# Kernel optimization log

Measured on AMD Instinct MI355X. Metric: run time of the kernel, lower is better.

## Reference

```python
import jax, jax.numpy as jnp
import numpy as np

SPLIT = 8            # square window (split_size=[8,8], idx 0/1 identical)
DIM = 192
HEADS = 8
NH = HEADS // 2      # heads per branch
CH = DIM // 2        # channels per branch
HD = CH // NH        # head dim = 24
POS_DIM = (CH // 4) // 4  # DynamicPosBias hidden = 6
SCALE = HD ** -0.5
N = SPLIT * SPLIT    # window token count = 64


def _rel_index():
    c = np.arange(SPLIT)
    coords = np.stack(np.meshgrid(c, c, indexing='ij')).reshape(2, -1)
    rel = (coords[:, :, None] - coords[:, None, :]).transpose(1, 2, 0)
    rel[:, :, 0] += SPLIT - 1
    rel[:, :, 1] += SPLIT - 1
    rel[:, :, 0] *= 2 * SPLIT - 1
    return rel.sum(-1).reshape(-1)  # (N*N,) in [0, (2*SPLIT-1)^2)


def _rpe_biases():
    h = np.arange(1 - SPLIT, SPLIT)
    b = np.stack(np.meshgrid(h, h, indexing='ij')).reshape(2, -1).T
    return b.astype(np.float32)  # ((2*SPLIT-1)^2, 2) = (225, 2)


def _layernorm(x, g, b):
    mu = x.mean(-1, keepdims=True)
    var = ((x - mu) ** 2).mean(-1, keepdims=True)
    return (x - mu) / jnp.sqrt(var + 1e-5) * g + b


def setup_inputs() -> dict:
    key = jax.random.key(0)
    ks = jax.random.split(key, 12)
    s = 0.02
    inp = {
        'x': jax.random.normal(ks[0], (2, 65536, DIM), jnp.float32),
        'qkv_w': jax.random.normal(ks[1], (3 * DIM, DIM), jnp.float32) * s,
        'proj_w': jax.random.normal(ks[2], (DIM, DIM), jnp.float32) * s,
        'proj_b': jnp.zeros((DIM,), jnp.float32),
        # DynamicPosBias params, stacked over the 2 branches
        'pos_proj_w': jax.random.normal(ks[3], (2, POS_DIM, 2), jnp.float32) * s,
        'pos_proj_b': jnp.zeros((2, POS_DIM), jnp.float32),
        'ln1_g': jnp.ones((2, POS_DIM), jnp.float32),
        'ln1_b': jnp.zeros((2, POS_DIM), jnp.float32),
        'fc1_w': jax.random.normal(ks[4], (2, POS_DIM, POS_DIM), jnp.float32) * s,
        'fc1_b': jnp.zeros((2, POS_DIM), jnp.float32),
        'ln2_g': jnp.ones((2, POS_DIM), jnp.float32),
        'ln2_b': jnp.zeros((2, POS_DIM), jnp.float32),
        'fc2_w': jax.random.normal(ks[5], (2, POS_DIM, POS_DIM), jnp.float32) * s,
        'fc2_b': jnp.zeros((2, POS_DIM), jnp.float32),
        'ln3_g': jnp.ones((2, POS_DIM), jnp.float32),
        'ln3_b': jnp.zeros((2, POS_DIM), jnp.float32),
        'fc3_w': jax.random.normal(ks[6], (2, NH, POS_DIM), jnp.float32) * s,
        'fc3_b': jnp.zeros((2, NH), jnp.float32),
        'H': 256,
        'W': 256,
    }
    return inp


def reference(x, qkv_w, proj_w, proj_b, pos_proj_w, pos_proj_b,
              ln1_g, ln1_b, fc1_w, fc1_b, ln2_g, ln2_b, fc2_w, fc2_b,
              ln3_g, ln3_b, fc3_w, fc3_b, H, W):
    B, L, C = x.shape
    assert L == H * W and H % SPLIT == 0 and W % SPLIT == 0
    qkv = (x @ qkv_w.T).reshape(B, L, 3, C).transpose(2, 0, 1, 3)  # (3,B,L,C)
    rel_idx = jnp.asarray(_rel_index())
    rpe = jnp.asarray(_rpe_biases())
    outs = []
    for i in range(2):  # two channel-split branches
        qkv_i = qkv[..., i * CH:(i + 1) * CH]  # (3,B,L,CH)
        # window partition: (B,L,CH) -> (B*nW, NH, N, HD)
        def im2win(t):
            t = t.reshape(B, H // SPLIT, SPLIT, W // SPLIT, SPLIT, CH)
            t = t.transpose(0, 1, 3, 2, 4, 5).reshape(-1, N, NH, HD)
            return t.transpose(0, 2, 1, 3)
        q, k, v = im2win(qkv_i[0]), im2win(qkv_i[1]), im2win(qkv_i[2])
        attn = jnp.einsum('whnd,whmd->whnm', q * SCALE, k)  # (B*nW, NH, N, N)
        # dynamic relative position bias MLP (residual=False): pos3(pos2(pos1(proj(b))))
        pos = rpe @ pos_proj_w[i].T + pos_proj_b[i]
        pos = jax.nn.relu(_layernorm(pos, ln1_g[i], ln1_b[i])) @ fc1_w[i].T + fc1_b[i]
        pos = jax.nn.relu(_layernorm(pos, ln2_g[i], ln2_b[i])) @ fc2_w[i].T + fc2_b[i]
        pos = jax.nn.relu(_layernorm(pos, ln3_g[i], ln3_b[i])) @ fc3_w[i].T + fc3_b[i]  # (225, NH)
        bias = pos[rel_idx].reshape(N, N, NH).transpose(2, 0, 1)  # (NH, N, N)
        attn = jax.nn.softmax(attn + bias[None], axis=-1)
        o = jnp.einsum('whnm,whmd->whnd', attn, v)  # (B*nW, NH, N, HD)
        # windows2img back to (B, L, CH)
        o = o.transpose(0, 2, 1, 3).reshape(B, H // SPLIT, W // SPLIT, SPLIT, SPLIT, CH)
        o = o.transpose(0, 1, 3, 2, 4, 5).reshape(B, L, CH)
        outs.append(o)
    out = jnp.concatenate(outs, axis=-1)
    return out @ proj_w.T + proj_b
```

## Files before the change

### kernel.cpp

```cpp
#include <hip/hip_runtime.h>

typedef unsigned short u16;
typedef short short8v __attribute__((ext_vector_type(8)));
typedef float float4v __attribute__((ext_vector_type(4)));
typedef unsigned short ushort4v __attribute__((ext_vector_type(4)));

#define XLD   216
#define C1LD  392
#define VSLD  72
#define PLD   72
#define VS_OFF (64*C1LD)
#define LDS_U16 (VS_OFF + 8*24*VSLD)
#define LDS_BYTES (LDS_U16*2)

__device__ __forceinline__ u16 f2bf(float f){
  unsigned u = __builtin_bit_cast(unsigned, f);
  return (u16)((u + 0x7FFFu + ((u >> 16) & 1u)) >> 16);
}

__global__ void prep_convert(const float* __restrict__ qkv_w, const float* __restrict__ proj_w,
                             u16* __restrict__ Wq, u16* __restrict__ Wp){
  int idx = blockIdx.x*blockDim.x + threadIdx.x;
  const int total = 110592 + 36864;
  for (; idx < total; idx += gridDim.x*blockDim.x){
    if (idx < 110592) Wq[idx] = f2bf(qkv_w[idx]);
    else              Wp[idx-110592] = f2bf(proj_w[idx-110592]);
  }
}

__device__ __forceinline__ void lnrelu6(float* v, const float* g, const float* b){
  float mu = (v[0]+v[1]+v[2]+v[3]+v[4]+v[5]) * (1.0f/6.0f);
  float var = 0.f;
  #pragma unroll
  for (int j=0;j<6;++j){ float d = v[j]-mu; var += d*d; }
  var *= (1.0f/6.0f);
  float inv = rsqrtf(var + 1e-5f);
  #pragma unroll
  for (int j=0;j<6;++j) v[j] = fmaxf((v[j]-mu)*inv*g[j] + b[j], 0.f);
}

__global__ void prep_bias(const float* __restrict__ ppw, const float* __restrict__ ppb,
                          const float* __restrict__ ln1g, const float* __restrict__ ln1b,
                          const float* __restrict__ fc1w, const float* __restrict__ fc1b,
                          const float* __restrict__ ln2g, const float* __restrict__ ln2b,
                          const float* __restrict__ fc2w, const float* __restrict__ fc2b,
                          const float* __restrict__ ln3g, const float* __restrict__ ln3b,
                          const float* __restrict__ fc3w, const float* __restrict__ fc3b,
                          float* __restrict__ biasT){
  __shared__ float pos3[2][225][4];
  const int t = threadIdx.x;
  if (t < 225){
    const float dy = (float)(t/15) - 7.0f;
    const float dx = (float)(t%15) - 7.0f;
    for (int i=0;i<2;++i){
      float v[6], y[6];
      #pragma unroll
      for (int j=0;j<6;++j)
        v[j] = dy*ppw[(i*6+j)*2+0] + dx*ppw[(i*6+j)*2+1] + ppb[i*6+j];
      lnrelu6(v, ln1g+i*6, ln1b+i*6);
      #pragma unroll
      for (int j=0;j<6;++j){
        float a = fc1b[i*6+j];
        #pragma unroll
        for (int k=0;k<6;++k) a += v[k]*fc1w[(i*6+j)*6+k];
        y[j] = a;
      }
      lnrelu6(y, ln2g+i*6, ln2b+i*6);
      #pragma unroll
      for (int j=0;j<6;++j){
        float a = fc2b[i*6+j];
        #pragma unroll
        for (int k=0;k<6;++k) a += y[k]*fc2w[(i*6+j)*6+k];
        v[j] = a;
      }
      lnrelu6(v, ln3g+i*6, ln3b+i*6);
      #pragma unroll
      for (int h=0;h<4;++h){
        float a = fc3b[i*4+h];
        #pragma unroll
        for (int k=0;k<6;++k) a += v[k]*fc3w[(i*4+h)*6+k];
        pos3[i][t][h] = a;
      }
    }
  }
  __syncthreads();
  for (int idx = t; idx < 32768; idx += 256){
    int i  = idx >> 14;
    int hh = (idx >> 12) & 3;
    int n  = (idx >> 6) & 63;
    int m  = idx & 63;
    int tt = (((n>>3)-(m>>3)+7)*15) + ((n&7)-(m&7)+7);
    biasT[idx] = pos3[i][tt][hh];
  }
}

__global__ __launch_bounds__(256, 2) void awa_main(
    const float* __restrict__ x, const u16* __restrict__ Wq,
    const u16* __restrict__ Wp, const float* __restrict__ proj_b,
    const float* __restrict__ biasT, float* __restrict__ out){
  extern __shared__ u16 lds[];
  const int tid  = threadIdx.x;
  const int wave = tid >> 6;
  const int lane = tid & 63;
  const int g    = lane >> 4;
  const int q16  = lane & 15;
  const int bid  = blockIdx.x;
  const int b    = bid >> 10;
  const int win  = bid & 1023;
  const int h1   = win >> 5, w1 = win & 31;
  const size_t xbase = ((size_t)b*65536u + (size_t)(h1*8)*256u + (size_t)(w1*8)) * 192u;
  const short8v z8 = {0,0,0,0,0,0,0,0};

  #pragma unroll
  for (int it = 0; it < 12; ++it){
    int fi  = tid + it*256;
    int f   = fi << 2;
    int rr  = f / 1536;
    int rem = f - rr*1536;
    int ss  = rem / 192;
    int cc  = rem - ss*192;
    float4v xv = *(const float4v*)(x + xbase + (size_t)((rr*256 + ss)*192 + cc));
    ushort4v pk = { f2bf(xv[0]), f2bf(xv[1]), f2bf(xv[2]), f2bf(xv[3]) };
    *(ushort4v*)&lds[(rr*8+ss)*XLD + cc] = pk;
  }
  __syncthreads();

  short8v xf[4][6];
  #pragma unroll
  for (int mt=0; mt<4; ++mt)
    #pragma unroll
    for (int kc=0; kc<6; ++kc)
      xf[mt][kc] = *(const short8v*)&lds[(mt*16+q16)*XLD + kc*32 + g*8];
  short8v wf[2][6];
  {
    const u16* wb = Wq + (size_t)(wave*16 + q16)*192 + g*8;
    #pragma unroll
    for (int kc=0;kc<6;++kc) wf[0][kc] = *(const short8v*)(wb + kc*32);
  }
  __syncthreads();

  #pragma unroll
  for (int t=0; t<9; ++t){
    const int nt = wave + t*4;
    if (t < 8){
      const u16* wb = Wq + (size_t)((nt+4)*16 + q16)*192 + g*8;
      #pragma unroll
      for (int kc=0;kc<6;++kc) wf[(t+1)&1][kc] = *(const short8v*)(wb + kc*32);
    }
    float4v acc[4];
    #pragma unroll
    for (int mt=0;mt<4;++mt) acc[mt] = (float4v){0.f,0.f,0.f,0.f};
    if (t < 6){
      #pragma unroll
      for (int kc=0; kc<6; ++kc)
        #pragma unroll
        for (int mt=0; mt<4; ++mt)
          acc[mt] = __builtin_amdgcn_mfma_f32_16x16x32_bf16(wf[t&1][kc], xf[mt][kc], acc[mt], 0,0,0);
      const int cb = nt*16 + g*4;
      #pragma unroll
      for (int mt=0; mt<4; ++mt){
        ushort4v pk = { f2bf(acc[mt][0]), f2bf(acc[mt][1]), f2bf(acc[mt][2]), f2bf(acc[mt][3]) };
        *(ushort4v*)&lds[(mt*16+q16)*C1LD + cb] = pk;
      }
    } else {
      #pragma unroll
      for (int kc=0; kc<6; ++kc)
        #pragma unroll
        for (int mt=0; mt<4; ++mt)
          acc[mt] = __builtin_amdgcn_mfma_f32_16x16x32_bf16(xf[mt][kc], wf[t&1][kc], acc[mt], 0,0,0);
      const int jj  = nt*16 + q16 - 384;
      const int ii2 = (jj >= 96) ? 1 : 0;
      const int c2  = jj - ii2*96;
      const int hh2 = c2 / 24;
      const int d   = c2 - hh2*24;
      const int vb  = VS_OFF + ((ii2*4 + hh2)*24 + d)*VSLD + g*4;
      #pragma unroll
      for (int mt=0; mt<4; ++mt){
        ushort4v pk = { f2bf(acc[mt][0]), f2bf(acc[mt][1]), f2bf(acc[mt][2]), f2bf(acc[mt][3]) };
        *(ushort4v*)&lds[vb + mt*16] = pk;
      }
    }
  }
  __syncthreads();

  short8v qf[2][4], kf[2][4];
  #pragma unroll
  for (int h=0; h<2; ++h){
    const int qb = h*96 + wave*24;
    #pragma unroll
    for (int mt=0; mt<4; ++mt){
      short8v a = *(const short8v*)&lds[(mt*16+q16)*C1LD + qb + g*8];
      short8v c = *(const short8v*)&lds[(mt*16+q16)*C1LD + 192 + qb + g*8];
      qf[h][mt] = (g==3) ? z8 : a;
      kf[h][mt] = (g==3) ? z8 : c;
    }
  }
  __syncthreads();

  u16* P = &lds[wave*4608];
  float4v oo[2][2][4];
  #pragma unroll
  for (int h=0; h<2; ++h){
    const int hp = h*4 + wave;
    float4v s[4][4];
    #pragma unroll
    for (int kt=0;kt<4;++kt)
      #pragma unroll
      for (int mt=0;mt<4;++mt)
        s[kt][mt] = (float4v){0.f,0.f,0.f,0.f};
    #pragma unroll
    for (int kt=0;kt<4;++kt)
      #pragma unroll
      for (int mt=0;mt<4;++mt)
        s[kt][mt] = __builtin_amdgcn_mfma_f32_16x16x32_bf16(kf[h][kt], qf[h][mt], s[kt][mt], 0,0,0);
    const float* bt = biasT + hp*4096;
    #pragma unroll
    for (int kt=0;kt<4;++kt)
      #pragma unroll
      for (int mt=0;mt<4;++mt){
        float4v bv = *(const float4v*)&bt[(mt*16+q16)*64 + kt*16 + g*4];
        s[kt][mt] = s[kt][mt]*0.20412414523193154f + bv;
      }
    #pragma unroll
    for (int mt=0;mt<4;++mt){
      float mx = s[0][mt][0];
      #pragma unroll
      for (int kt=0;kt<4;++kt)
        #pragma unroll
        for (int r=0;r<4;++r) mx = fmaxf(mx, s[kt][mt][r]);
      mx = fmaxf(mx, __shfl_xor(mx, 16));
      mx = fmaxf(mx, __shfl_xor(mx, 32));
      float e[4][4]; float sum = 0.f;
      #pragma unroll
      for (int kt=0;kt<4;++kt)
        #pragma unroll
        for (int r=0;r<4;++r){ float t2 = __expf(s[kt][mt][r]-mx); e[kt][r] = t2; sum += t2; }
      sum += __shfl_xor(sum, 16);
      sum += __shfl_xor(sum, 32);
      const float inv = 1.0f / sum;
      #pragma unroll
      for (int kt=0;kt<4;++kt){
        ushort4v pk = { f2bf(e[kt][0]*inv), f2bf(e[kt][1]*inv), f2bf(e[kt][2]*inv), f2bf(e[kt][3]*inv) };
        *(ushort4v*)&P[(mt*16+q16)*PLD + kt*16 + g*4] = pk;
      }
    }
    short8v vf[2][2];
    #pragma unroll
    for (int dt=0;dt<2;++dt){
      const int d  = dt*16 + q16;
      const int dc = (d < 24) ? d : 0;
      #pragma unroll
      for (int kc=0;kc<2;++kc){
        short8v vv = *(const short8v*)&lds[VS_OFF + (hp*24 + dc)*VSLD + kc*32 + g*8];
        vf[dt][kc] = (d < 24) ? vv : z8;
      }
    }
    #pragma unroll
    for (int dt=0;dt<2;++dt)
      #pragma unroll
      for (int mt=0;mt<4;++mt) oo[h][dt][mt] = (float4v){0.f,0.f,0.f,0.f};
    #pragma unroll
    for (int mt=0;mt<4;++mt){
      #pragma unroll
      for (int kc=0;kc<2;++kc){
        short8v pf = *(const short8v*)&P[(mt*16+q16)*PLD + kc*32 + g*8];
        #pragma unroll
        for (int dt=0;dt<2;++dt)
          oo[h][dt][mt] = __builtin_amdgcn_mfma_f32_16x16x32_bf16(vf[dt][kc], pf, oo[h][dt][mt], 0,0,0);
      }
    }
  }
  __syncthreads();

  #pragma unroll
  for (int h=0; h<2; ++h){
    const int cb = h*96 + wave*24;
    #pragma unroll
    for (int dt=0; dt<2; ++dt){
      if (dt==0 || g<2){
        #pragma unroll
        for (int mt=0; mt<4; ++mt){
          ushort4v pk = { f2bf(oo[h][dt][mt][0]), f2bf(oo[h][dt][mt][1]),
                          f2bf(oo[h][dt][mt][2]), f2bf(oo[h][dt][mt][3]) };
          *(ushort4v*)&lds[(mt*16+q16)*XLD + cb + dt*16 + g*4] = pk;
        }
      }
    }
  }
  short8v wp[2][6];
  {
    const u16* wb = Wp + (size_t)(wave*16 + q16)*192 + g*8;
    #pragma unroll
    for (int kc=0;kc<6;++kc) wp[0][kc] = *(const short8v*)(wb + kc*32);
  }
  __syncthreads();

  short8v a2[4][6];
  #pragma unroll
  for (int mt=0; mt<4; ++mt)
    #pragma unroll
    for (int kc=0; kc<6; ++kc)
      a2[mt][kc] = *(const short8v*)&lds[(mt*16+q16)*XLD + kc*32 + g*8];
  #pragma unroll
  for (int t=0; t<3; ++t){
    const int nt = wave + t*4;
    if (t < 2){
      const u16* wb = Wp + (size_t)((nt+4)*16 + q16)*192 + g*8;
      #pragma unroll
      for (int kc=0;kc<6;++kc) wp[(t+1)&1][kc] = *(const short8v*)(wb + kc*32);
    }
    float4v acc[4];
    #pragma unroll
    for (int mt=0;mt<4;++mt) acc[mt] = (float4v){0.f,0.f,0.f,0.f};
    #pragma unroll
    for (int kc=0; kc<6; ++kc)
      #pragma unroll
      for (int mt=0; mt<4; ++mt)
        acc[mt] = __builtin_amdgcn_mfma_f32_16x16x32_bf16(wp[t&1][kc], a2[mt][kc], acc[mt], 0,0,0);
    const int j0 = nt*16 + g*4;
    const float4v pb = *(const float4v*)(proj_b + j0);
    #pragma unroll
    for (int mt=0; mt<4; ++mt){
      const int tok = mt*16 + q16;
      const int l = ((h1*8 + (tok>>3)) << 8) + w1*8 + (tok & 7);
      float4v res = acc[mt] + pb;
      *(float4v*)(out + ((size_t)b*65536u + (size_t)l)*192u + j0) = res;
    }
  }
}

extern "C" void kernel_launch(void* const* d_in, const int* in_sizes, int n_in,
                              void* d_out, int out_size, void* d_ws, size_t ws_size,
                              hipStream_t stream){
  const float* x      = (const float*)d_in[0];
  const float* qkv_w  = (const float*)d_in[1];
  const float* proj_w = (const float*)d_in[2];
  const float* proj_b = (const float*)d_in[3];
  const float* ppw    = (const float*)d_in[4];
  const float* ppb    = (const float*)d_in[5];
  const float* ln1g   = (const float*)d_in[6];
  const float* ln1b   = (const float*)d_in[7];
  const float* fc1w   = (const float*)d_in[8];
  const float* fc1b   = (const float*)d_in[9];
  const float* ln2g   = (const float*)d_in[10];
  const float* ln2b   = (const float*)d_in[11];
  const float* fc2w   = (const float*)d_in[12];
  const float* fc2b   = (const float*)d_in[13];
  const float* ln3g   = (const float*)d_in[14];
  const float* ln3b   = (const float*)d_in[15];
  const float* fc3w   = (const float*)d_in[16];
  const float* fc3b   = (const float*)d_in[17];

  u16*   Wq    = (u16*)d_ws;
  u16*   Wp    = Wq + 110592;
  float* biasT = (float*)((char*)d_ws + 294912);

  prep_convert<<<144, 256, 0, stream>>>(qkv_w, proj_w, Wq, Wp);
  prep_bias<<<1, 256, 0, stream>>>(ppw, ppb, ln1g, ln1b, fc1w, fc1b,
                                   ln2g, ln2b, fc2w, fc2b, ln3g, ln3b,
                                   fc3w, fc3b, biasT);
  awa_main<<<2048, 256, LDS_BYTES, stream>>>(x, Wq, Wp, proj_b, biasT, (float*)d_out);
}
```

Baseline: 143.1 us.

## Use eight waves per window block, one head per wave, with MFMA priority hints

Result: slower. 196.4 us (+37.2%).

```diff
diff --git a/kernel.cpp b/kernel.cpp
--- a/kernel.cpp
+++ b/kernel.cpp
@@ -94,7 +94,7 @@
   }
 }
 
-__global__ __launch_bounds__(256, 2) void awa_main(
+__global__ __launch_bounds__(512, 4) void awa_main(
     const float* __restrict__ x, const u16* __restrict__ Wq,
     const u16* __restrict__ Wp, const float* __restrict__ proj_b,
     const float* __restrict__ biasT, float* __restrict__ out){
@@ -104,6 +104,8 @@
   const int lane = tid & 63;
   const int g    = lane >> 4;
   const int q16  = lane & 15;
+  const int mh   = wave & 1;
+  const int ng   = wave >> 1;
   const int bid  = blockIdx.x;
   const int b    = bid >> 10;
   const int win  = bid & 1023;
@@ -112,8 +114,8 @@
   const short8v z8 = {0,0,0,0,0,0,0,0};
 
   #pragma unroll
-  for (int it = 0; it < 12; ++it){
-    int fi  = tid + it*256;
+  for (int it = 0; it < 6; ++it){
+    int fi  = tid + it*512;
     int f   = fi << 2;
     int rr  = f / 1536;
     int rem = f - rr*1536;
@@ -125,15 +127,15 @@
   }
   __syncthreads();
 
-  short8v xf[4][6];
-  #pragma unroll
-  for (int mt=0; mt<4; ++mt)
+  short8v xf[2][6];
+  #pragma unroll
+  for (int mi=0; mi<2; ++mi)
     #pragma unroll
     for (int kc=0; kc<6; ++kc)
-      xf[mt][kc] = *(const short8v*)&lds[(mt*16+q16)*XLD + kc*32 + g*8];
+      xf[mi][kc] = *(const short8v*)&lds[((mh*2+mi)*16+q16)*XLD + kc*32 + g*8];
   short8v wf[2][6];
   {
-    const u16* wb = Wq + (size_t)(wave*16 + q16)*192 + g*8;
+    const u16* wb = Wq + (size_t)(ng*16 + q16)*192 + g*8;
     #pragma unroll
     for (int kc=0;kc<6;++kc) wf[0][kc] = *(const short8v*)(wb + kc*32);
   }
@@ -141,33 +143,33 @@
 
   #pragma unroll
   for (int t=0; t<9; ++t){
-    const int nt = wave + t*4;
+    const int nt = ng + t*4;
     if (t < 8){
       const u16* wb = Wq + (size_t)((nt+4)*16 + q16)*192 + g*8;
       #pragma unroll
       for (int kc=0;kc<6;++kc) wf[(t+1)&1][kc] = *(const short8v*)(wb + kc*32);
     }
-    float4v acc[4];
-    #pragma unroll
-    for (int mt=0;mt<4;++mt) acc[mt] = (float4v){0.f,0.f,0.f,0.f};
+    float4v acc[2];
+    acc[0] = (float4v){0.f,0.f,0.f,0.f};
+    acc[1] = (float4v){0.f,0.f,0.f,0.f};
     if (t < 6){
       #pragma unroll
       for (int kc=0; kc<6; ++kc)
         #pragma unroll
-        for (int mt=0; mt<4; ++mt)
-          acc[mt] = __builtin_amdgcn_mfma_f32_16x16x32_bf16(wf[t&1][kc], xf[mt][kc], acc[mt], 0,0,0);
+        for (int mi=0; mi<2; ++mi)
+          acc[mi] = __builtin_amdgcn_mfma_f32_16x16x32_bf16(wf[t&1][kc], xf[mi][kc], acc[mi], 0,0,0);
       const int cb = nt*16 + g*4;
       #pragma unroll
-      for (int mt=0; mt<4; ++mt){
-        ushort4v pk = { f2bf(acc[mt][0]), f2bf(acc[mt][1]), f2bf(acc[mt][2]), f2bf(acc[mt][3]) };
-        *(ushort4v*)&lds[(mt*16+q16)*C1LD + cb] = pk;
+      for (int mi=0; mi<2; ++mi){
+        ushort4v pk = { f2bf(acc[mi][0]), f2bf(acc[mi][1]), f2bf(acc[mi][2]), f2bf(acc[mi][3]) };
+        *(ushort4v*)&lds[((mh*2+mi)*16+q16)*C1LD + cb] = pk;
       }
     } else {
       #pragma unroll
       for (int kc=0; kc<6; ++kc)
         #pragma unroll
-        for (int mt=0; mt<4; ++mt)
-          acc[mt] = __builtin_amdgcn_mfma_f32_16x16x32_bf16(xf[mt][kc], wf[t&1][kc], acc[mt], 0,0,0);
+        for (int mi=0; mi<2; ++mi)
+          acc[mi] = __builtin_amdgcn_mfma_f32_16x16x32_bf16(xf[mi][kc], wf[t&1][kc], acc[mi], 0,0,0);
       const int jj  = nt*16 + q16 - 384;
       const int ii2 = (jj >= 96) ? 1 : 0;
       const int c2  = jj - ii2*96;
@@ -175,44 +177,53 @@
       const int d   = c2 - hh2*24;
       const int vb  = VS_OFF + ((ii2*4 + hh2)*24 + d)*VSLD + g*4;
       #pragma unroll
-      for (int mt=0; mt<4; ++mt){
-        ushort4v pk = { f2bf(acc[mt][0]), f2bf(acc[mt][1]), f2bf(acc[mt][2]), f2bf(acc[mt][3]) };
-        *(ushort4v*)&lds[vb + mt*16] = pk;
-      }
-    }
-  }
-  __syncthreads();
-
-  short8v qf[2][4], kf[2][4];
-  #pragma unroll
-  for (int h=0; h<2; ++h){
-    const int qb = h*96 + wave*24;
-    #pragma unroll
-    for (int mt=0; mt<4; ++mt){
-      short8v a = *(const short8v*)&lds[(mt*16+q16)*C1LD + qb + g*8];
-      short8v c = *(const short8v*)&lds[(mt*16+q16)*C1LD + 192 + qb + g*8];
-      qf[h][mt] = (g==3) ? z8 : a;
-      kf[h][mt] = (g==3) ? z8 : c;
+      for (int mi=0; mi<2; ++mi){
+        ushort4v pk = { f2bf(acc[mi][0]), f2bf(acc[mi][1]), f2bf(acc[mi][2]), f2bf(acc[mi][3]) };
+        *(ushort4v*)&lds[vb + (mh*2+mi)*16] = pk;
+      }
+    }
+  }
+  __syncthreads();
+
+  const int hp = wave;
+  const int qb = (hp>>2)*96 + (hp&3)*24;
+  short8v qf[4], kf[4];
+  #pragma unroll
+  for (int mt=0; mt<4; ++mt){
+    short8v a = *(const short8v*)&lds[(mt*16+q16)*C1LD + qb + g*8];
+    short8v c = *(const short8v*)&lds[(mt*16+q16)*C1LD + 192 + qb + g*8];
+    qf[mt] = (g==3) ? z8 : a;
+    kf[mt] = (g==3) ? z8 : c;
+  }
+  short8v vf[2][2];
+  #pragma unroll
+  for (int dt=0;dt<2;++dt){
+    const int d  = dt*16 + q16;
+    const int dc = (d < 24) ? d : 0;
+    #pragma unroll
+    for (int kc=0;kc<2;++kc){
+      short8v vv = *(const short8v*)&lds[VS_OFF + (hp*24 + dc)*VSLD + kc*32 + g*8];
+      vf[dt][kc] = (d < 24) ? vv : z8;
     }
   }
   __syncthreads();
 
   u16* P = &lds[wave*4608];
-  float4v oo[2][2][4];
-  #pragma unroll
-  for (int h=0; h<2; ++h){
-    const int hp = h*4 + wave;
+  float4v oo[2][4];
+  {
     float4v s[4][4];
     #pragma unroll
     for (int kt=0;kt<4;++kt)
       #pragma unroll
       for (int mt=0;mt<4;++mt)
         s[kt][mt] = (float4v){0.f,0.f,0.f,0.f};
+    __builtin_amdgcn_s_setprio(1);
     #pragma unroll
     for (int kt=0;kt<4;++kt)
       #pragma unroll
       for (int mt=0;mt<4;++mt)
-        s[kt][mt] = __builtin_amdgcn_mfma_f32_16x16x32_bf16(kf[h][kt], qf[h][mt], s[kt][mt], 0,0,0);
+        s[kt][mt] = __builtin_amdgcn_mfma_f32_16x16x32_bf16(kf[kt], qf[mt], s[kt][mt], 0,0,0);
+    __builtin_amdgcn_s_setprio(0);
     const float* bt = biasT + hp*4096;
     #pragma unroll
     for (int kt=0;kt<4;++kt)
@@ -244,86 +255,79 @@
         *(ushort4v*)&P[(mt*16+q16)*PLD + kt*16 + g*4] = pk;
       }
     }
-    short8v vf[2][2];
-    #pragma unroll
-    for (int dt=0;dt<2;++dt){
-      const int d  = dt*16 + q16;
-      const int dc = (d < 24) ? d : 0;
-      #pragma unroll
-      for (int kc=0;kc<2;++kc){
-        short8v vv = *(const short8v*)&lds[VS_OFF + (hp*24 + dc)*VSLD + kc*32 + g*8];
-        vf[dt][kc] = (d < 24) ? vv : z8;
-      }
-    }
     #pragma unroll
     for (int dt=0;dt<2;++dt)
       #pragma unroll
-      for (int mt=0;mt<4;++mt) oo[h][dt][mt] = (float4v){0.f,0.f,0.f,0.f};
+      for (int mt=0;mt<4;++mt) oo[dt][mt] = (float4v){0.f,0.f,0.f,0.f};
     #pragma unroll
     for (int mt=0;mt<4;++mt){
       #pragma unroll
       for (int kc=0;kc<2;++kc){
         short8v pf = *(const short8v*)&P[(mt*16+q16)*PLD + kc*32 + g*8];
+        __builtin_amdgcn_s_setprio(1);
         #pragma unroll
         for (int dt=0;dt<2;++dt)
-          oo[h][dt][mt] = __builtin_amdgcn_mfma_f32_16x16x32_bf16(vf[dt][kc], pf, oo[h][dt][mt], 0,0,0);
-      }
-    }
-  }
-  __syncthreads();
-
-  #pragma unroll
-  for (int h=0; h<2; ++h){
-    const int cb = h*96 + wave*24;
+          oo[dt][mt] = __builtin_amdgcn_mfma_f32_16x16x32_bf16(vf[dt][kc], pf, oo[dt][mt], 0,0,0);
+        __builtin_amdgcn_s_setprio(0);
+      }
+    }
+  }
+  __syncthreads();
+
+  {
+    const int cb = qb;
     #pragma unroll
     for (int dt=0; dt<2; ++dt){
       if (dt==0 || g<2){
         #pragma unroll
         for (int mt=0; mt<4; ++mt){
-          ushort4v pk = { f2bf(oo[h][dt][mt][0]), f2bf(oo[h][dt][mt][1]),
-                          f2bf(oo[h][dt][mt][2]), f2bf(oo[h][dt][mt][3]) };
+          ushort4v pk = { f2bf(oo[dt][mt][0]), f2bf(oo[dt][mt][1]),
+                          f2bf(oo[dt][mt][2]), f2bf(oo[dt][mt][3]) };
           *(ushort4v*)&lds[(mt*16+q16)*XLD + cb + dt*16 + g*4] = pk;
         }
       }
     }
   }
+  const int nq = wave >> 1;
   short8v wp[2][6];
   {
-    const u16* wb = Wp + (size_t)(wave*16 + q16)*192 + g*8;
+    const u16* wb = Wp + (size_t)(nq*16 + q16)*192 + g*8;
     #pragma unroll
     for (int kc=0;kc<6;++kc) wp[0][kc] = *(const short8v*)(wb + kc*32);
   }
   __syncthreads();
 
-  short8v a2[4][6];
-  #pragma unroll
-  for (int mt=0; mt<4; ++mt)
+  short8v a2[2][6];
+  #pragma unroll
+  for (int mi=0; mi<2; ++mi)
     #pragma unroll
     for (int kc=0; kc<6; ++kc)
-      a2[mt][kc] = *(const short8v*)&lds[(mt*16+q16)*XLD + kc*32 + g*8];
+      a2[mi][kc] = *(const short8v*)&lds[((mh*2+mi)*16+q16)*XLD + kc*32 + g*8];
   #pragma unroll
   for (int t=0; t<3; ++t){
-    const int nt = wave + t*4;
+    const int nt = nq + t*4;
     if (t < 2){
       const u16* wb = Wp + (size_t)((nt+4)*16 + q16)*192 + g*8;
       #pragma unroll
       for (int kc=0;kc<6;++kc) wp[(t+1)&1][kc] = *(const short8v*)(wb + kc*32);
     }
-    float4v acc[4];
-    #pragma unroll
-    for (int mt=0;mt<4;++mt) acc[mt] = (float4v){0.f,0.f,0.f,0.f};
+    float4v acc[2];
+    acc[0] = (float4v){0.f,0.f,0.f,0.f};
+    acc[1] = (float4v){0.f,0.f,0.f,0.f};
+    __builtin_amdgcn_s_setprio(1);
     #pragma unroll
     for (int kc=0; kc<6; ++kc)
       #pragma unroll
-      for (int mt=0; mt<4; ++mt)
-        acc[mt] = __builtin_amdgcn_mfma_f32_16x16x32_bf16(wp[t&1][kc], a2[mt][kc], acc[mt], 0,0,0);
+      for (int mi=0; mi<2; ++mi)
+        acc[mi] = __builtin_amdgcn_mfma_f32_16x16x32_bf16(wp[t&1][kc], a2[mi][kc], acc[mi], 0,0,0);
+    __builtin_amdgcn_s_setprio(0);
     const int j0 = nt*16 + g*4;
     const float4v pb = *(const float4v*)(proj_b + j0);
     #pragma unroll
-    for (int mt=0; mt<4; ++mt){
-      const int tok = mt*16 + q16;
+    for (int mi=0; mi<2; ++mi){
+      const int tok = (mh*2+mi)*16 + q16;
       const int l = ((h1*8 + (tok>>3)) << 8) + w1*8 + (tok & 7);
-      float4v res = acc[mt] + pb;
+      float4v res = acc[mi] + pb;
       *(float4v*)(out + ((size_t)b*65536u + (size_t)l)*192u + j0) = res;
     }
   }
@@ -359,5 +363,5 @@
   prep_bias<<<1, 256, 0, stream>>>(ppw, ppb, ln1g, ln1b, fc1w, fc1b,
                                    ln2g, ln2b, fc2w, fc2b, ln3g, ln3b,
                                    fc3w, fc3b, biasT);
-  awa_main<<<2048, 256, LDS_BYTES, stream>>>(x, Wq, Wp, proj_b, biasT, (float*)d_out);
-}
+  awa_main<<<2048, 512, LDS_BYTES, stream>>>(x, Wq, Wp, proj_b, biasT, (float*)d_out);
+}
```

## Process four windows per block with register prefetch of next window input

Applied to the files above, without the earlier changes.

New measurement: 224.7 us. 1.57x slower.

```diff
diff --git a/kernel.cpp b/kernel.cpp
--- a/kernel.cpp
+++ b/kernel.cpp
@@ -12,6 +12,9 @@
 #define VS_OFF (64*C1LD)
 #define LDS_U16 (VS_OFF + 8*24*VSLD)
 #define LDS_BYTES (LDS_U16*2)
+
+#define SOFT_BAR() do { asm volatile("s_waitcnt lgkmcnt(0)" ::: "memory"); \
+                        __builtin_amdgcn_s_barrier(); } while(0)
 
 __device__ __forceinline__ u16 f2bf(float f){
   unsigned u = __builtin_bit_cast(unsigned, f);
@@ -94,6 +97,81 @@
   }
 }
 
+__device__ __forceinline__ void attn_head(u16* lds, u16* P, const float* bt,
+                                          const short8v* qf, const short8v* kf,
+                                          const float4v* bv, int hp, int q16, int g,
+                                          float4v (&oo)[2][4]){
+  const short8v z8 = {0,0,0,0,0,0,0,0};
+  float4v s[4][4];
+  #pragma unroll
+  for (int kt=0;kt<4;++kt)
+    #pragma unroll
+    for (int mt=0;mt<4;++mt)
+      s[kt][mt] = (float4v){0.f,0.f,0.f,0.f};
+  __builtin_amdgcn_s_setprio(1);
+  #pragma unroll
+  for (int kt=0;kt<4;++kt)
+    #pragma unroll
+    for (int mt=0;mt<4;++mt)
+      s[kt][mt] = __builtin_amdgcn_mfma_f32_16x16x32_bf16(kf[kt], qf[mt], s[kt][mt], 0,0,0);
+  __builtin_amdgcn_s_setprio(0);
+  #pragma unroll
+  for (int kt=0;kt<4;++kt)
+    #pragma unroll
+    for (int mt=0;mt<4;++mt)
+      s[kt][mt] = s[kt][mt]*0.20412414523193154f + bv[kt*4+mt];
+  #pragma unroll
+  for (int mt=0;mt<4;++mt){
+    float mx = s[0][mt][0];
+    #pragma unroll
+    for (int kt=0;kt<4;++kt)
+      #pragma unroll
+      for (int r=0;r<4;++r) mx = fmaxf(mx, s[kt][mt][r]);
+    mx = fmaxf(mx, __shfl_xor(mx, 16));
+    mx = fmaxf(mx, __shfl_xor(mx, 32));
+    float e[4][4]; float sum = 0.f;
+    #pragma unroll
+    for (int kt=0;kt<4;++kt)
+      #pragma unroll
+      for (int r=0;r<4;++r){ float t2 = __expf(s[kt][mt][r]-mx); e[kt][r] = t2; sum += t2; }
+    sum += __shfl_xor(sum, 16);
+    sum += __shfl_xor(sum, 32);
+    const float inv = 1.0f / sum;
+    #pragma unroll
+    for (int kt=0;kt<4;++kt){
+      ushort4v pk = { f2bf(e[kt][0]*inv), f2bf(e[kt][1]*inv), f2bf(e[kt][2]*inv), f2bf(e[kt][3]*inv) };
+      *(ushort4v*)&P[(mt*16+q16)*PLD + kt*16 + g*4] = pk;
+    }
+  }
+  short8v vf[2][2];
+  #pragma unroll
+  for (int dt=0;dt<2;++dt){
+    const int d  = dt*16 + q16;
+    const int dc = (d < 24) ? d : 0;
+    #pragma unroll
+    for (int kc=0;kc<2;++kc){
+      short8v vv = *(const short8v*)&lds[VS_OFF + (hp*24 + dc)*VSLD + kc*32 + g*8];
+      vf[dt][kc] = (d < 24) ? vv : z8;
+    }
+  }
+  #pragma unroll
+  for (int dt=0;dt<2;++dt)
+    #pragma unroll
+    for (int mt=0;mt<4;++mt) oo[dt][mt] = (float4v){0.f,0.f,0.f,0.f};
+  #pragma unroll
+  for (int mt=0;mt<4;++mt){
+    #pragma unroll
+    for (int kc=0;kc<2;++kc){
+      short8v pf = *(const short8v*)&P[(mt*16+q16)*PLD + kc*32 + g*8];
+      __builtin_amdgcn_s_setprio(1);
+      #pragma unroll
+      for (int dt=0;dt<2;++dt)
+        oo[dt][mt] = __builtin_amdgcn_mfma_f32_16x16x32_bf16(vf[dt][kc], pf, oo[dt][mt], 0,0,0);
+      __builtin_amdgcn_s_setprio(0);
+    }
+  }
+}
+
 __global__ __launch_bounds__(256, 2) void awa_main(
     const float* __restrict__ x, const u16* __restrict__ Wq,
     const u16* __restrict__ Wp, const float* __restrict__ proj_b,
@@ -104,228 +182,202 @@
   const int lane = tid & 63;
   const int g    = lane >> 4;
   const int q16  = lane & 15;
-  const int bid  = blockIdx.x;
-  const int b    = bid >> 10;
-  const int win  = bid & 1023;
-  const int h1   = win >> 5, w1 = win & 31;
-  const size_t xbase = ((size_t)b*65536u + (size_t)(h1*8)*256u + (size_t)(w1*8)) * 192u;
   const short8v z8 = {0,0,0,0,0,0,0,0};
 
-  #pragma unroll
-  for (int it = 0; it < 12; ++it){
-    int fi  = tid + it*256;
-    int f   = fi << 2;
-    int rr  = f / 1536;
-    int rem = f - rr*1536;
-    int ss  = rem / 192;
-    int cc  = rem - ss*192;
-    float4v xv = *(const float4v*)(x + xbase + (size_t)((rr*256 + ss)*192 + cc));
-    ushort4v pk = { f2bf(xv[0]), f2bf(xv[1]), f2bf(xv[2]), f2bf(xv[3]) };
-    *(ushort4v*)&lds[(rr*8+ss)*XLD + cc] = pk;
-  }
-  __syncthreads();
-
-  short8v xf[4][6];
-  #pragma unroll
-  for (int mt=0; mt<4; ++mt)
-    #pragma unroll
-    for (int kc=0; kc<6; ++kc)
-      xf[mt][kc] = *(const short8v*)&lds[(mt*16+q16)*XLD + kc*32 + g*8];
-  short8v wf[2][6];
+  float4v xr[12];
+  int gw = blockIdx.x*4;
   {
-    const u16* wb = Wq + (size_t)(wave*16 + q16)*192 + g*8;
-    #pragma unroll
-    for (int kc=0;kc<6;++kc) wf[0][kc] = *(const short8v*)(wb + kc*32);
-  }
-  __syncthreads();
-
-  #pragma unroll
-  for (int t=0; t<9; ++t){
-    const int nt = wave + t*4;
-    if (t < 8){
-      const u16* wb = Wq + (size_t)((nt+4)*16 + q16)*192 + g*8;
-      #pragma unroll
-      for (int kc=0;kc<6;++kc) wf[(t+1)&1][kc] = *(const short8v*)(wb + kc*32);
-    }
-    float4v acc[4];
-    #pragma unroll
-    for (int mt=0;mt<4;++mt) acc[mt] = (float4v){0.f,0.f,0.f,0.f};
-    if (t < 6){
+    const int b0 = gw >> 10, win0 = gw & 1023;
+    const size_t xb = ((size_t)b0*65536u + (size_t)((win0>>5)*8)*256u + (size_t)((win0&31)*8)) * 192u;
+    #pragma unroll
+    for (int it=0; it<12; ++it){
+      int f = (tid + it*256) << 2;
+      int rr = f/1536, rem = f - rr*1536, ss = rem/192, cc = rem - ss*192;
+      xr[it] = *(const float4v*)(x + xb + (size_t)((rr*256+ss)*192+cc));
+    }
+  }
+
+  for (int wloc = 0; wloc < 4; ++wloc){
+    const int b   = gw >> 10;
+    const int win = gw & 1023;
+    const int h1  = win >> 5, w1 = win & 31;
+
+    #pragma unroll
+    for (int it=0; it<12; ++it){
+      int f = (tid + it*256) << 2;
+      int rr = f/1536, rem = f - rr*1536, ss = rem/192, cc = rem - ss*192;
+      ushort4v pk = { f2bf(xr[it][0]), f2bf(xr[it][1]), f2bf(xr[it][2]), f2bf(xr[it][3]) };
+      *(ushort4v*)&lds[(rr*8+ss)*XLD + cc] = pk;
+    }
+    SOFT_BAR();
+
+    short8v xf[4][6];
+    #pragma unroll
+    for (int mt=0; mt<4; ++mt)
       #pragma unroll
       for (int kc=0; kc<6; ++kc)
+        xf[mt][kc] = *(const short8v*)&lds[(mt*16+q16)*XLD + kc*32 + g*8];
+    short8v wf[2][6];
+    {
+      const u16* wb = Wq + (size_t)(wave*16 + q16)*192 + g*8;
+      #pragma unroll
+      for (int kc=0;kc<6;++kc) wf[0][kc] = *(const short8v*)(wb + kc*32);
+    }
+    SOFT_BAR();
+
+    #pragma unroll
+    for (int t=0; t<9; ++t){
+      const int nt = wave + t*4;
+      if (t < 8){
+        const u16* wb = Wq + (size_t)((nt+4)*16 + q16)*192 + g*8;
+        #pragma unroll
+        for (int kc=0;kc<6;++kc) wf[(t+1)&1][kc] = *(const short8v*)(wb + kc*32);
+      }
+      float4v acc[4];
+      #pragma unroll
+      for (int mt=0;mt<4;++mt) acc[mt] = (float4v){0.f,0.f,0.f,0.f};
+      if (t < 6){
+        #pragma unroll
+        for (int kc=0; kc<6; ++kc)
+          #pragma unroll
+          for (int mt=0; mt<4; ++mt)
+            acc[mt] = __builtin_amdgcn_mfma_f32_16x16x32_bf16(wf[t&1][kc], xf[mt][kc], acc[mt], 0,0,0);
+        const int cb = nt*16 + g*4;
+        #pragma unroll
+        for (int mt=0; mt<4; ++mt){
+          ushort4v pk = { f2bf(acc[mt][0]), f2bf(acc[mt][1]), f2bf(acc[mt][2]), f2bf(acc[mt][3]) };
+          *(ushort4v*)&lds[(mt*16+q16)*C1LD + cb] = pk;
+        }
+      } else {
+        #pragma unroll
+        for (int kc=0; kc<6; ++kc)
+          #pragma unroll
+          for (int mt=0; mt<4; ++mt)
+            acc[mt] = __builtin_amdgcn_mfma_f32_16x16x32_bf16(xf[mt][kc], wf[t&1][kc], acc[mt], 0,0,0);
+        const int jj  = nt*16 + q16 - 384;
+        const int ii2 = (jj >= 96) ? 1 : 0;
+        const int c2  = jj - ii2*96;
+        const int hh2 = c2 / 24;
+        const int d   = c2 - hh2*24;
+        const int vb  = VS_OFF + ((ii2*4 + hh2)*24 + d)*VSLD + g*4;
+        #pragma unroll
+        for (int mt=0; mt<4; ++mt){
+          ushort4v pk = { f2bf(acc[mt][0]), f2bf(acc[mt][1]), f2bf(acc[mt][2]), f2bf(acc[mt][3]) };
+          *(ushort4v*)&lds[vb + mt*16] = pk;
+        }
+      }
+    }
+    SOFT_BAR();
+
+    short8v qf[2][4], kf[2][4];
+    #pragma unroll
+    for (int h=0; h<2; ++h){
+      const int qb = h*96 + wave*24;
+      #pragma unroll
+      for (int mt=0; mt<4; ++mt){
+        short8v a = *(const short8v*)&lds[(mt*16+q16)*C1LD + qb + g*8];
+        short8v c = *(const short8v*)&lds[(mt*16+q16)*C1LD + 192 + qb + g*8];
+        qf[h][mt] = (g==3) ? z8 : a;
+        kf[h][mt] = (g==3) ? z8 : c;
+      }
+    }
+    float4v bv0[16];
+    {
+      const float* bt = biasT + wave*4096;
+      #pragma unroll
+      for (int kt=0;kt<4;++kt)
+        #pragma unroll
+        for (int mt=0;mt<4;++mt)
+          bv0[kt*4+mt] = *(const float4v*)&bt[(mt*16+q16)*64 + kt*16 + g*4];
+    }
+    SOFT_BAR();
+
+    u16* P = &lds[wave*4608];
+    float4v oo0[2][4], oo1[2][4];
+    attn_head(lds, P, biasT, qf[0], kf[0], bv0, wave, q16, g, oo0);
+    float4v bv1[16];
+    {
+      const float* bt = biasT + (4+wave)*4096;
+      #pragma unroll
+      for (int kt=0;kt<4;++kt)
+        #pragma unroll
+        for (int mt=0;mt<4;++mt)
+          bv1[kt*4+mt] = *(const float4v*)&bt[(mt*16+q16)*64 + kt*16 + g*4];
+    }
+    attn_head(lds, P, biasT, qf[1], kf[1], bv1, 4+wave, q16, g, oo1);
+    SOFT_BAR();
+
+    if (wloc < 3){
+      const int gwn = gw + 1;
+      const int bn = gwn >> 10, winn = gwn & 1023;
+      const size_t xbn = ((size_t)bn*65536u + (size_t)((winn>>5)*8)*256u + (size_t)((winn&31)*8)) * 192u;
+      #pragma unroll
+      for (int it=0; it<12; ++it){
+        int f = (tid + it*256) << 2;
+        int rr = f/1536, rem = f - rr*1536, ss = rem/192, cc = rem - ss*192;
+        xr[it] = *(const float4v*)(x + xbn + (size_t)((rr*256+ss)*192+cc));
+      }
+    }
+    #pragma unroll
+    for (int h=0; h<2; ++h){
+      const int cb = h*96 + wave*24;
+      float4v (&oo)[2][4] = (h==0) ? oo0 : oo1;
+      #pragma unroll
+      for (int dt=0; dt<2; ++dt){
+        if (dt==0 || g<2){
+          #pragma unroll
+          for (int mt=0; mt<4; ++mt){
+            ushort4v pk = { f2bf(oo[dt][mt][0]), f2bf(oo[dt][mt][1]),
+                            f2bf(oo[dt][mt][2]), f2bf(oo[dt][mt][3]) };
+            *(ushort4v*)&lds[(mt*16+q16)*XLD + cb + dt*16 + g*4] = pk;
+          }
+        }
+      }
+    }
+    short8v wp[2][6];
+    {
+      const u16* wb = Wp + (size_t)(wave*16 + q16)*192 + g*8;
+      #pragma unroll
+      for (int kc=0;kc<6;++kc) wp[0][kc] = *(const short8v*)(wb + kc*32);
+    }
+    SOFT_BAR();
+
+    short8v a2[4][6];
+    #pragma unroll
+    for (int mt=0; mt<4; ++mt)
+      #pragma unroll
+      for (int kc=0; kc<6; ++kc)
+        a2[mt][kc] = *(const short8v*)&lds[(mt*16+q16)*XLD + kc*32 + g*8];
+    #pragma unroll
+    for (int t=0; t<3; ++t){
+      const int nt = wave + t*4;
+      if (t < 2){
+        const u16* wb = Wp + (size_t)((nt+4)*16 + q16)*192 + g*8;
+        #pragma unroll
+        for (int kc=0;kc<6;++kc) wp[(t+1)&1][kc] = *(const short8v*)(wb + kc*32);
+      }
+      float4v acc[4];
+      #pragma unroll
+      for (int mt=0;mt<4;++mt) acc[mt] = (float4v){0.f,0.f,0.f,0.f};
+      __builtin_amdgcn_s_setprio(1);
+      #pragma unroll
+      for (int kc=0; kc<6; ++kc)
         #pragma unroll
         for (int mt=0; mt<4; ++mt)
-          acc[mt] = __builtin_amdgcn_mfma_f32_16x16x32_bf16(wf[t&1][kc], xf[mt][kc], acc[mt], 0,0,0);
-      const int cb = nt*16 + g*4;
+          acc[mt] = __builtin_amdgcn_mfma_f32_16x16x32_bf16(wp[t&1][kc], a2[mt][kc], acc[mt], 0,0,0);
+      __builtin_amdgcn_s_setprio(0);
+      const int j0 = nt*16 + g*4;
+      const float4v pb = *(const float4v*)(proj_b + j0);
       #pragma unroll
       for (int mt=0; mt<4; ++mt){
-        ushort4v pk = { f2bf(acc[mt][0]), f2bf(acc[mt][1]), f2bf(acc[mt][2]), f2bf(acc[mt][3]) };
-        *(ushort4v*)&lds[(mt*16+q16)*C1LD + cb] = pk;
-      }
-    } else {
-      #pragma unroll
-      for (int kc=0; kc<6; ++kc)
-        #pragma unroll
-        for (int mt=0; mt<4; ++mt)
-          acc[mt] = __builtin_amdgcn_mfma_f32_16x16x32_bf16(xf[mt][kc], wf[t&1][kc], acc[mt], 0,0,0);
-      const int jj  = nt*16 + q16 - 384;
-      const int ii2 = (jj >= 96) ? 1 : 0;
-      const int c2  = jj - ii2*96;
-      const int hh2 = c2 / 24;
-      const int d   = c2 - hh2*24;
-      const int vb  = VS_OFF + ((ii2*4 + hh2)*24 + d)*VSLD + g*4;
-      #pragma unroll
-      for (int mt=0; mt<4; ++mt){
-        ushort4v pk = { f2bf(acc[mt][0]), f2bf(acc[mt][1]), f2bf(acc[mt][2]), f2bf(acc[mt][3]) };
-        *(ushort4v*)&lds[vb + mt*16] = pk;
-      }
-    }
-  }
-  __syncthreads();
-
-  short8v qf[2][4], kf[2][4];
-  #pragma unroll
-  for (int h=0; h<2; ++h){
-    const int qb = h*96 + wave*24;
-    #pragma unroll
-    for (int mt=0; mt<4; ++mt){
-      short8v a = *(const short8v*)&lds[(mt*16+q16)*C1LD + qb + g*8];
-      short8v c = *(const short8v*)&lds[(mt*16+q16)*C1LD + 192 + qb + g*8];
-      qf[h][mt] = (g==3) ? z8 : a;
-      kf[h][mt] = (g==3) ? z8 : c;
-    }
-  }
-  __syncthreads();
-
-  u16* P = &lds[wave*4608];
-  float4v oo[2][2][4];
-  #pragma unroll
-  for (int h=0; h<2; ++h){
-    const int hp = h*4 + wave;
-    float4v s[4][4];
-    #pragma unroll
-    for (int kt=0;kt<4;++kt)
-      #pragma unroll
-      for (int mt=0;mt<4;++mt)
-        s[kt][mt] = (float4v){0.f,0.f,0.f,0.f};
-    #pragma unroll
-    for (int kt=0;kt<4;++kt)
-      #pragma unroll
-      for (int mt=0;mt<4;++mt)
-        s[kt][mt] = __builtin_amdgcn_mfma_f32_16x16x32_bf16(kf[h][kt], qf[h][mt], s[kt][mt], 0,0,0);
-    const float* bt = biasT + hp*4096;
-    #pragma unroll
-    for (int kt=0;kt<4;++kt)
-      #pragma unroll
-      for (int mt=0;mt<4;++mt){
-        float4v bv = *(const float4v*)&bt[(mt*16+q16)*64 + kt*16 + g*4];
-        s[kt][mt] = s[kt][mt]*0.20412414523193154f + bv;
-      }
-    #pragma unroll
-    for (int mt=0;mt<4;++mt){
-      float mx = s[0][mt][0];
-      #pragma unroll
-      for (int kt=0;kt<4;++kt)
-        #pragma unroll
-        for (int r=0;r<4;++r) mx = fmaxf(mx, s[kt][mt][r]);
-      mx = fmaxf(mx, __shfl_xor(mx, 16));
-      mx = fmaxf(mx, __shfl_xor(mx, 32));
-      float e[4][4]; float sum = 0.f;
-      #pragma unroll
-      for (int kt=0;kt<4;++kt)
-        #pragma unroll
-        for (int r=0;r<4;++r){ float t2 = __expf(s[kt][mt][r]-mx); e[kt][r] = t2; sum += t2; }
-      sum += __shfl_xor(sum, 16);
-      sum += __shfl_xor(sum, 32);
-      const float inv = 1.0f / sum;
-      #pragma unroll
-      for (int kt=0;kt<4;++kt){
-        ushort4v pk = { f2bf(e[kt][0]*inv), f2bf(e[kt][1]*inv), f2bf(e[kt][2]*inv), f2bf(e[kt][3]*inv) };
-        *(ushort4v*)&P[(mt*16+q16)*PLD + kt*16 + g*4] = pk;
-      }
-    }
-    short8v vf[2][2];
-    #pragma unroll
-    for (int dt=0;dt<2;++dt){
-      const int d  = dt*16 + q16;
-      const int dc = (d < 24) ? d : 0;
-      #pragma unroll
-      for (int kc=0;kc<2;++kc){
-        short8v vv = *(const short8v*)&lds[VS_OFF + (hp*24 + dc)*VSLD + kc*32 + g*8];
-        vf[dt][kc] = (d < 24) ? vv : z8;
-      }
-    }
-    #pragma unroll
-    for (int dt=0;dt<2;++dt)
-      #pragma unroll
-      for (int mt=0;mt<4;++mt) oo[h][dt][mt] = (float4v){0.f,0.f,0.f,0.f};
-    #pragma unroll
-    for (int mt=0;mt<4;++mt){
-      #pragma unroll
-      for (int kc=0;kc<2;++kc){
-        short8v pf = *(const short8v*)&P[(mt*16+q16)*PLD + kc*32 + g*8];
-        #pragma unroll
-        for (int dt=0;dt<2;++dt)
-          oo[h][dt][mt] = __builtin_amdgcn_mfma_f32_16x16x32_bf16(vf[dt][kc], pf, oo[h][dt][mt], 0,0,0);
-      }
-    }
-  }
-  __syncthreads();
-
-  #pragma unroll
-  for (int h=0; h<2; ++h){
-    const int cb = h*96 + wave*24;
-    #pragma unroll
-    for (int dt=0; dt<2; ++dt){
-      if (dt==0 || g<2){
-        #pragma unroll
-        for (int mt=0; mt<4; ++mt){
-          ushort4v pk = { f2bf(oo[h][dt][mt][0]), f2bf(oo[h][dt][mt][1]),
-                          f2bf(oo[h][dt][mt][2]), f2bf(oo[h][dt][mt][3]) };
-          *(ushort4v*)&lds[(mt*16+q16)*XLD + cb + dt*16 + g*4] = pk;
-        }
-      }
-    }
-  }
-  short8v wp[2][6];
-  {
-    const u16* wb = Wp + (size_t)(wave*16 + q16)*192 + g*8;
-    #pragma unroll
-    for (int kc=0;kc<6;++kc) wp[0][kc] = *(const short8v*)(wb + kc*32);
-  }
-  __syncthreads();
-
-  short8v a2[4][6];
-  #pragma unroll
-  for (int mt=0; mt<4; ++mt)
-    #pragma unroll
-    for (int kc=0; kc<6; ++kc)
-      a2[mt][kc] = *(const short8v*)&lds[(mt*16+q16)*XLD + kc*32 + g*8];
-  #pragma unroll
-  for (int t=0; t<3; ++t){
-    const int nt = wave + t*4;
-    if (t < 2){
-      const u16* wb = Wp + (size_t)((nt+4)*16 + q16)*192 + g*8;
-      #pragma unroll
-      for (int kc=0;kc<6;++kc) wp[(t+1)&1][kc] = *(const short8v*)(wb + kc*32);
-    }
-    float4v acc[4];
-    #pragma unroll
-    for (int mt=0;mt<4;++mt) acc[mt] = (float4v){0.f,0.f,0.f,0.f};
-    #pragma unroll
-    for (int kc=0; kc<6; ++kc)
-      #pragma unroll
-      for (int mt=0; mt<4; ++mt)
-        acc[mt] = __builtin_amdgcn_mfma_f32_16x16x32_bf16(wp[t&1][kc], a2[mt][kc], acc[mt], 0,0,0);
-    const int j0 = nt*16 + g*4;
-    const float4v pb = *(const float4v*)(proj_b + j0);
-    #pragma unroll
-    for (int mt=0; mt<4; ++mt){
-      const int tok = mt*16 + q16;
-      const int l = ((h1*8 + (tok>>3)) << 8) + w1*8 + (tok & 7);
-      float4v res = acc[mt] + pb;
-      *(float4v*)(out + ((size_t)b*65536u + (size_t)l)*192u + j0) = res;
-    }
+        const int tok = mt*16 + q16;
+        const int l = ((h1*8 + (tok>>3)) << 8) + w1*8 + (tok & 7);
+        float4v res = acc[mt] + pb;
+        *(float4v*)(out + ((size_t)b*65536u + (size_t)l)*192u + j0) = res;
+      }
+    }
+    ++gw;
+    if (wloc < 3) SOFT_BAR();
   }
 }
 
@@ -359,5 +411,5 @@
   prep_bias<<<1, 256, 0, stream>>>(ppw, ppb, ln1g, ln1b, fc1w, fc1b,
                                    ln2g, ln2b, fc2w, fc2b, ln3g, ln3b,
                                    fc3w, fc3b, biasT);
-  awa_main<<<2048, 256, LDS_BYTES, stream>>>(x, Wq, Wp, proj_b, biasT, (float*)d_out);
-}
+  awa_main<<<512, 256, LDS_BYTES, stream>>>(x, Wq, Wp, proj_b, biasT, (float*)d_out);
+}
```
